# Kernel tuning notes

Measured on AMD Instinct MI355X. Metric: run time of the kernel, lower is better.

Reference implementation:

```python
import jax, jax.numpy as jnp
import numpy as np

NUM_HEADS = 12
TOP_K = 2
ROPE_THETA = 10000.0
EPS = 1e-6

def _rmsnorm(x, w):
    return x * jax.lax.rsqrt(jnp.mean(x * x, axis=-1, keepdims=True) + EPS) * w

def _rotate_half(t):
    t1, t2 = jnp.split(t, 2, axis=-1)
    return jnp.concatenate([-t2, t1], axis=-1)

def setup_inputs() -> dict:
    key = jax.random.key(0)
    ks = jax.random.split(key, 8)
    B, S, H, E, F = 2, 2048, 768, 8, 3072
    s = 0.02
    return {
        "x": jax.random.normal(ks[0], (B, S, H), dtype=jnp.float32),
        "attn_norm_w": jnp.ones((H,), dtype=jnp.float32),
        "wqkv": jax.random.normal(ks[1], (H, 3 * H), dtype=jnp.float32) * s,
        "wo": jax.random.normal(ks[2], (H, H), dtype=jnp.float32) * s,
        "ffn_norm_w": jnp.ones((H,), dtype=jnp.float32),
        "router_w": jax.random.normal(ks[3], (H, E), dtype=jnp.float32) * s,
        "w1": jax.random.normal(ks[4], (E, H, F), dtype=jnp.float32) * s,
        "w2": jax.random.normal(ks[5], (E, F, H), dtype=jnp.float32) * s,
    }

def reference(x, attn_norm_w, wqkv, wo, ffn_norm_w, router_w, w1, w2):
    B, S, H = x.shape
    NH, Dh = NUM_HEADS, H // NUM_HEADS
    E = router_w.shape[1]

    # ---- attention sub-block: x = x + attn(rmsnorm(x)) ----
    h = _rmsnorm(x, attn_norm_w)
    qkv = h @ wqkv  # (B,S,3H)
    q, k, v = [t.reshape(B, S, NH, Dh) for t in jnp.split(qkv, 3, axis=-1)]

    # RoPE (llama-style half-split rotation)
    half = Dh // 2
    inv_freq = 1.0 / (ROPE_THETA ** (jnp.arange(half, dtype=jnp.float32) / half))
    ang = jnp.arange(S, dtype=jnp.float32)[:, None] * inv_freq[None, :]  # (S, half)
    cos = jnp.concatenate([jnp.cos(ang)] * 2, axis=-1)[None, :, None, :].astype(x.dtype)
    sin = jnp.concatenate([jnp.sin(ang)] * 2, axis=-1)[None, :, None, :].astype(x.dtype)
    q = q * cos + _rotate_half(q) * sin
    k = k * cos + _rotate_half(k) * sin

    scores = jnp.einsum('bqhd,bkhd->bhqk', q, k) / jnp.sqrt(jnp.asarray(Dh, x.dtype))
    causal = jnp.tril(jnp.ones((S, S), dtype=bool))
    scores = jnp.where(causal[None, None], scores, jnp.asarray(-1e9, x.dtype))
    attn = jax.nn.softmax(scores, axis=-1)
    o = jnp.einsum('bhqk,bkhd->bqhd', attn, v).reshape(B, S, H) @ wo
    x = x + o

    # ---- MoE FFN sub-block: x = x + moe(rmsnorm(x)) ----
    hn = _rmsnorm(x, ffn_norm_w).reshape(-1, H)  # (T,H)
    logits = hn @ router_w  # (T,E)
    probs = jax.nn.softmax(logits, axis=-1)
    top_v, top_i = jax.lax.top_k(probs, TOP_K)  # (T,K)
    top_v = top_v / jnp.sum(top_v, axis=-1, keepdims=True)
    onehot = jax.nn.one_hot(top_i, E, dtype=x.dtype)  # (T,K,E)
    combine = jnp.einsum('tke,tk->te', onehot, top_v)  # (T,E)

    h1 = jnp.einsum('th,ehf->etf', hn, w1)
    h2 = jnp.einsum('etf,efh->eth', jax.nn.silu(h1), w2)
    moe_out = jnp.einsum('eth,te->th', h2, combine).reshape(B, S, H)

    # load-balancing aux loss (switch-style)
    frac = jnp.mean(jnp.sum(onehot, axis=1), axis=0) / TOP_K  # (E,)
    mean_prob = jnp.mean(probs, axis=0)  # (E,)
    aux = jnp.asarray(E, x.dtype) * jnp.sum(frac * mean_prob)

    return (x + moe_out, aux)
```

## Files before the change

### kernel.cpp

```cpp
#include <hip/hip_runtime.h>
#include <cstdint>
#include <cstddef>

typedef __bf16 bf16;
typedef bf16 bf16x8 __attribute__((ext_vector_type(8)));
typedef bf16 bf16x4 __attribute__((ext_vector_type(4)));
typedef float f32x4 __attribute__((ext_vector_type(4)));

static constexpr size_t SKS = (size_t)10240 * 768;

template <int N> struct ICst { static constexpr int v = N; };

__device__ __forceinline__ void async_cp16(const void* g, void* l) {
    __builtin_amdgcn_global_load_lds(
        (const __attribute__((address_space(1))) unsigned int*)(unsigned long long)g,
        (__attribute__((address_space(3))) unsigned int*)(unsigned int)(unsigned long long)l,
        16, 0, 0);
}

#define BARX() __builtin_amdgcn_s_barrier()
#define LGKM0() asm volatile("s_waitcnt lgkmcnt(0)" ::: "memory")
#define VMC8() asm volatile("s_waitcnt vmcnt(8)" ::: "memory")
#define VMC0() asm volatile("s_waitcnt vmcnt(0)" ::: "memory")

__device__ __forceinline__ void tc_body(const float* __restrict__ in, bf16* __restrict__ out,
                                        int R, int C, int r0, int c0, float* shf) {
    float (*tile)[33] = (float(*)[33])shf;
    int tid = threadIdx.x;
    int lr = tid >> 3, lc = (tid & 7) * 4;
    float4 v = *(const float4*)&in[(size_t)(r0 + lr) * C + c0 + lc];
    tile[lr][lc] = v.x; tile[lr][lc + 1] = v.y; tile[lr][lc + 2] = v.z; tile[lr][lc + 3] = v.w;
    __syncthreads();
    int sc = tid >> 3, sr = (tid & 7) * 4;
    bf16x4 o;
    o[0] = (bf16)tile[sr][sc]; o[1] = (bf16)tile[sr + 1][sc];
    o[2] = (bf16)tile[sr + 2][sc]; o[3] = (bf16)tile[sr + 3][sc];
    *(bf16x4*)&out[(size_t)(c0 + sc) * R + r0 + sr] = o;
}

__global__ __launch_bounds__(256) void prep1(const float* __restrict__ x,
                                             const float* __restrict__ anw,
                                             bf16* __restrict__ hbuf,
                                             const float* __restrict__ wqkv,
                                             bf16* __restrict__ wqkvT,
                                             const float* __restrict__ wo,
                                             bf16* __restrict__ woT,
                                             int* __restrict__ ctrl) {
    __shared__ __align__(16) float shf[32 * 33];
    const int bid = (int)blockIdx.x, tid = threadIdx.x;
    if (bid < 4096) {
        const float* xr = x + (size_t)bid * 768;
        float v0 = xr[tid], v1 = xr[tid + 256], v2 = xr[tid + 512];
        float s = v0 * v0 + v1 * v1 + v2 * v2;
#pragma unroll
        for (int off = 32; off; off >>= 1) s += __shfl_xor(s, off, 64);
        if ((tid & 63) == 0) shf[tid >> 6] = s;
        __syncthreads();
        float tot = shf[0] + shf[1] + shf[2] + shf[3];
        float rs = rsqrtf(tot * (1.f / 768.f) + 1e-6f);
        bf16* o = hbuf + (size_t)bid * 768;
        o[tid]       = (bf16)(v0 * rs * anw[tid]);
        o[tid + 256] = (bf16)(v1 * rs * anw[tid + 256]);
        o[tid + 512] = (bf16)(v2 * rs * anw[tid + 512]);
    } else if (bid < 5824) {
        int i = bid - 4096;
        tc_body(wqkv, wqkvT, 768, 2304, (i / 72) * 32, (i % 72) * 32, shf);
    } else if (bid < 6400) {
        int i = bid - 5824;
        tc_body(wo, woT, 768, 768, (i / 24) * 32, (i % 24) * 32, shf);
    } else {
        if (tid < 64) ctrl[tid] = 0;
    }
}

__global__ __launch_bounds__(256) void rope_kernel(const bf16* __restrict__ qkv,
                                                   bf16* __restrict__ qb,
                                                   bf16* __restrict__ kb,
                                                   bf16* __restrict__ vtb) {
    __shared__ float vs[64][65];
    const int tid = threadIdx.x;
    const int s0 = blockIdx.x * 64, bh = blockIdx.y;
    const int b = bh / 12, h = bh - b * 12;
    const float qscale = 0.18033688f;
#pragma unroll
    for (int i = 0; i < 16; ++i) {
        int idx = i * 256 + tid;
        int sl = idx >> 6, d = idx & 63;
        int sg = s0 + sl;
        size_t base = ((size_t)b * 2048 + sg) * 2304;
        float qv = (float)qkv[base + h * 64 + d];
        float kv = (float)qkv[base + 768 + h * 64 + d];
        float vv = (float)qkv[base + 1536 + h * 64 + d];
        float qp = (float)qkv[base + h * 64 + (d ^ 32)];
        float kp = (float)qkv[base + 768 + h * 64 + (d ^ 32)];
        int jj = d & 31;
        float invf = __expf(-(float)jj * (9.210340371976184f / 32.f));
        float ang = (float)sg * invf;
        float cv, sv;
        __sincosf(ang, &sv, &cv);
        float rq = (d < 32) ? -qp : qp;
        float rk = (d < 32) ? -kp : kp;
        qb[((size_t)bh * 2048 + sg) * 64 + d] = (bf16)((qv * cv + rq * sv) * qscale);
        kb[((size_t)bh * 2048 + sg) * 64 + d] = (bf16)(kv * cv + rk * sv);
        vs[sl][d] = vv;
    }
    __syncthreads();
#pragma unroll
    for (int i = 0; i < 16; ++i) {
        int idx = i * 256 + tid;
        int d = idx >> 6, sl = idx & 63;
        vtb[(size_t)bh * 64 * 2048 + (size_t)d * 2048 + s0 + sl] = (bf16)vs[sl][d];
    }
}

struct AttnSh {
    bf16 Qs[2][64][32];
    bf16 Ks[2][2][64][32];
    bf16 Vts[2][2][64][32];
    bf16 Ps[4][1024];
};
union ShU { AttnSh a; float tile[32 * 33]; };

__global__ __launch_bounds__(256) void attn_tw(const bf16* __restrict__ qb,
                                               const bf16* __restrict__ kb,
                                               const bf16* __restrict__ vtb,
                                               bf16* __restrict__ ob,
                                               const float* __restrict__ w1,
                                               bf16* __restrict__ w1T,
                                               const float* __restrict__ w2,
                                               bf16* __restrict__ w2T) {
    __shared__ __align__(16) ShU sh;
    const int bid = (int)blockIdx.x;

    if (bid >= 768) {
        int i = bid - 768;
        if (i < 18432) {
            int bz = i / 2304, r = i - bz * 2304;
            tc_body(w1 + (size_t)bz * 768 * 3072, w1T + (size_t)bz * 768 * 3072,
                    768, 3072, ((r / 96) % 24) * 32, (r % 96) * 32, sh.tile);
        } else {
            i -= 18432;
            int bz = i / 2304, r = i - bz * 2304;
            tc_body(w2 + (size_t)bz * 3072 * 768, w2T + (size_t)bz * 3072 * 768,
                    3072, 768, ((r / 24) % 96) * 32, (r % 24) * 32, sh.tile);
        }
        return;
    }

    const int tid = threadIdx.x, lane = tid & 63, w = tid >> 6;
    const int quad = lane >> 4, l16 = lane & 15;
    const int linear = bid;
    const int xcd = linear & 7, j = linear >> 3;
    const int bh = xcd * 3 + (j >> 5);
    const int qt = 31 - (j & 31);
    const int q0 = qt * 64;
    const int b = bh / 12, h = bh - b * 12;

    const bf16* qhead = qb + (size_t)bh * 2048 * 64;
    const bf16* khead = kb + (size_t)bh * 2048 * 64;
    const bf16* vthead = vtb + (size_t)bh * 64 * 2048;

#pragma unroll
    for (int i = 0; i < 2; ++i) {
        int o = (i * 256 + tid) * 16;
        int kk = o >> 12, row = (o >> 6) & 63, el = (o & 63) >> 1;
        async_cp16(qhead + (size_t)(q0 + row) * 64 + kk * 32 + el,
                   (char*)sh.a.Qs + (size_t)(i * 256 + w * 64) * 16);
    }
    __syncthreads();
    bf16x8 bq[2];
#pragma unroll
    for (int kk = 0; kk < 2; ++kk)
        bq[kk] = *(const bf16x8*)&sh.a.Qs[kk][w * 16 + l16][quad * 8];

    f32x4 o_acc[4] = {};
    float m_st = -1e30f, l_st = 0.f;

    for (int j2 = 0; j2 <= qt; j2 += 2) {
        int nt2 = (j2 + 1 <= qt) ? 2 : 1;
        __syncthreads();
#pragma unroll
        for (int t = 0; t < 2; ++t) {
            if (t >= nt2) break;
            int kv0 = (j2 + t) * 64;
#pragma unroll
            for (int i = 0; i < 2; ++i) {
                int o = (i * 256 + tid) * 16;
                int kk = o >> 12, row = (o >> 6) & 63, el = (o & 63) >> 1;
                async_cp16(khead + (size_t)(kv0 + row) * 64 + kk * 32 + el,
                           (char*)&sh.a.Ks[t] + (size_t)(i * 256 + w * 64) * 16);
                async_cp16(vthead + (size_t)row * 2048 + kv0 + kk * 32 + el,
                           (char*)&sh.a.Vts[t] + (size_t)(i * 256 + w * 64) * 16);
            }
        }
        __syncthreads();

#pragma unroll
        for (int t = 0; t < 2; ++t) {
            if (t >= nt2) break;

            f32x4 sacc[4] = {};
#pragma unroll
            for (int kk = 0; kk < 2; ++kk) {
                bf16x8 ak[4];
#pragma unroll
                for (int ni = 0; ni < 4; ++ni)
                    ak[ni] = *(const bf16x8*)&sh.a.Ks[t][kk][ni * 16 + l16][quad * 8];
#pragma unroll
                for (int ni = 0; ni < 4; ++ni)
                    sacc[ni] = __builtin_amdgcn_mfma_f32_16x16x32_bf16(ak[ni], bq[kk], sacc[ni], 0, 0, 0);
            }

            if (j2 + t == qt) {
                int ql = w * 16 + l16;
#pragma unroll
                for (int ni = 0; ni < 4; ++ni)
#pragma unroll
                    for (int r = 0; r < 4; ++r)
                        if (ni * 16 + quad * 4 + r > ql) sacc[ni][r] = -1e30f;
            }

            float mx = sacc[0][0];
#pragma unroll
            for (int ni = 0; ni < 4; ++ni)
#pragma unroll
                for (int r = 0; r < 4; ++r) mx = fmaxf(mx, sacc[ni][r]);
            mx = fmaxf(mx, __shfl_xor(mx, 16, 64));
            mx = fmaxf(mx, __shfl_xor(mx, 32, 64));
            float mnew = fmaxf(m_st, mx);
            float alpha = exp2f(m_st - mnew);
            m_st = mnew;
            float rsum = 0.f;
#pragma unroll
            for (int ni = 0; ni < 4; ++ni)
#pragma unroll
                for (int r = 0; r < 4; ++r) {
                    float pv = exp2f(sacc[ni][r] - mnew);
                    sacc[ni][r] = pv;
                    rsum += pv;
                }
            rsum += __shfl_xor(rsum, 16, 64);
            rsum += __shfl_xor(rsum, 32, 64);
            l_st = l_st * alpha + rsum;

            float af[4];
#pragma unroll
            for (int r = 0; r < 4; ++r) af[r] = __shfl(alpha, quad * 4 + r, 64);
#pragma unroll
            for (int ni = 0; ni < 4; ++ni)
#pragma unroll
                for (int r = 0; r < 4; ++r) o_acc[ni][r] *= af[r];

            bf16* pb = sh.a.Ps[w];
#pragma unroll
            for (int ni = 0; ni < 4; ++ni)
#pragma unroll
                for (int r = 0; r < 4; ++r) {
                    int kv = ni * 16 + quad * 4 + r;
                    int ch = (kv >> 3) ^ (l16 & 7);
                    pb[l16 * 64 + ch * 8 + (kv & 7)] = (bf16)sacc[ni][r];
                }

#pragma unroll
            for (int kk = 0; kk < 2; ++kk) {
                int ch = (kk * 4 + quad) ^ (l16 & 7);
                bf16x8 ap = *(const bf16x8*)&pb[l16 * 64 + ch * 8];
                bf16x8 bv[4];
#pragma unroll
                for (int ni = 0; ni < 4; ++ni)
                    bv[ni] = *(const bf16x8*)&sh.a.Vts[t][kk][ni * 16 + l16][quad * 8];
#pragma unroll
                for (int ni = 0; ni < 4; ++ni)
                    o_acc[ni] = __builtin_amdgcn_mfma_f32_16x16x32_bf16(ap, bv[ni], o_acc[ni], 0, 0, 0);
            }
        }
    }

    float lf[4];
#pragma unroll
    for (int r = 0; r < 4; ++r) lf[r] = 1.f / __shfl(l_st, quad * 4 + r, 64);
#pragma unroll
    for (int ni = 0; ni < 4; ++ni)
#pragma unroll
        for (int r = 0; r < 4; ++r) {
            int rowg = q0 + w * 16 + quad * 4 + r;
            size_t tk = (size_t)b * 2048 + rowg;
            ob[tk * 768 + h * 64 + ni * 16 + l16] = (bf16)(o_acc[ni][r] * lf[r]);
        }
}

__global__ __launch_bounds__(256) void rms_router(const float* __restrict__ x1,
                                                  const float* __restrict__ w,
                                                  const float* __restrict__ rw,
                                                  bf16* __restrict__ hn,
                                                  int* __restrict__ topi,
                                                  float* __restrict__ topw,
                                                  float* __restrict__ probsb) {
    __shared__ float hnf[768];
    __shared__ float part[256];
    __shared__ float lg[8];
    __shared__ float probs[8];
    __shared__ float red[4];
    int row = blockIdx.x, tid = threadIdx.x;
    const float* xr = x1 + (size_t)row * 768;
    float v0 = xr[tid], v1 = xr[tid + 256], v2 = xr[tid + 512];
    float s = v0 * v0 + v1 * v1 + v2 * v2;
#pragma unroll
    for (int off = 32; off; off >>= 1) s += __shfl_xor(s, off, 64);
    if ((tid & 63) == 0) red[tid >> 6] = s;
    __syncthreads();
    float tot = red[0] + red[1] + red[2] + red[3];
    float rs = rsqrtf(tot * (1.f / 768.f) + 1e-6f);
    float h0 = v0 * rs * w[tid], h1v = v1 * rs * w[tid + 256], h2v = v2 * rs * w[tid + 512];
    hnf[tid] = h0; hnf[tid + 256] = h1v; hnf[tid + 512] = h2v;
    bf16* o = hn + (size_t)row * 768;
    o[tid] = (bf16)h0; o[tid + 256] = (bf16)h1v; o[tid + 512] = (bf16)h2v;
    __syncthreads();
    int e = tid & 7, seg = tid >> 3;
    float p = 0.f;
#pragma unroll
    for (int j = 0; j < 24; ++j) { int k = seg * 24 + j; p += hnf[k] * rw[k * 8 + e]; }
    part[tid] = p;
    __syncthreads();
    if (tid < 8) { float a = 0.f; for (int sgi = 0; sgi < 32; ++sgi) a += part[sgi * 8 + tid]; lg[tid] = a; }
    __syncthreads();
    if (tid == 0) {
        float mx = lg[0];
        for (int i = 1; i < 8; ++i) mx = fmaxf(mx, lg[i]);
        float ssum = 0.f, ex[8];
        for (int i = 0; i < 8; ++i) { ex[i] = __expf(lg[i] - mx); ssum += ex[i]; }
        float inv = 1.f / ssum;
        for (int i = 0; i < 8; ++i) probs[i] = ex[i] * inv;
        int e0 = 0; float p0 = probs[0];
        for (int i = 1; i < 8; ++i) if (probs[i] > p0) { p0 = probs[i]; e0 = i; }
        int e1 = -1; float p1 = -1.f;
        for (int i = 0; i < 8; ++i) if (i != e0 && probs[i] > p1) { p1 = probs[i]; e1 = i; }
        float wsum = p0 + p1;
        topi[row * 2] = e0; topi[row * 2 + 1] = e1;
        topw[row * 2] = p0 / wsum; topw[row * 2 + 1] = p1 / wsum;
    }
    __syncthreads();
    if (tid < 8) probsb[(size_t)row * 8 + tid] = probs[tid];
}

__global__ __launch_bounds__(256) void router_stats(const float* __restrict__ probsb,
                                                    const int* __restrict__ topi,
                                                    int* ctrl, int4* tiles, float* auxOut) {
    __shared__ float pws[4][8];
    __shared__ int cws[4][8];
    int tid = threadIdx.x;
    float s[8] = {};
    int cnt[8] = {};
    for (int t = tid; t < 4096; t += 256) {
        const float4* p = (const float4*)(probsb + (size_t)t * 8);
        float4 a = p[0], b = p[1];
        s[0] += a.x; s[1] += a.y; s[2] += a.z; s[3] += a.w;
        s[4] += b.x; s[5] += b.y; s[6] += b.z; s[7] += b.w;
        int e0 = topi[2 * t], e1 = topi[2 * t + 1];
#pragma unroll
        for (int e = 0; e < 8; ++e) cnt[e] += (e == e0) + (e == e1);
    }
#pragma unroll
    for (int e = 0; e < 8; ++e)
#pragma unroll
        for (int off = 32; off; off >>= 1) {
            s[e] += __shfl_xor(s[e], off, 64);
            cnt[e] += __shfl_xor(cnt[e], off, 64);
        }
    if ((tid & 63) == 0) {
#pragma unroll
        for (int e = 0; e < 8; ++e) { pws[tid >> 6][e] = s[e]; cws[tid >> 6][e] = cnt[e]; }
    }
    __syncthreads();
    if (tid == 0) {
        int off = 0, nt = 0;
        float aux = 0.f;
        for (int e = 0; e < 8; ++e) {
            int ne = cws[0][e] + cws[1][e] + cws[2][e] + cws[3][e];
            float ps = pws[0][e] + pws[1][e] + pws[2][e] + pws[3][e];
            ctrl[e] = ne;
            ctrl[32 + e] = off;
            int ntl = (ne + 255) >> 8;
            for (int i = 0; i < ntl; ++i) { tiles[nt] = make_int4(e, off + i * 256, off + ne, 0); ++nt; }
            off += ntl << 8;
            aux += ((float)ne * (1.f / 8192.f)) * (ps * (1.f / 4096.f));
        }
        ctrl[24] = nt;
        auxOut[0] = 8.f * aux;
    }
}

__global__ __launch_bounds__(256) void place_tokens(const int* __restrict__ topi,
                                                    int* ctrl, int* __restrict__ perm,
                                                    int* __restrict__ tokslot) {
    __shared__ int lcnt[8], lbase[8];
    int tid = threadIdx.x;
    int t = blockIdx.x * 256 + tid;
    if (tid < 8) lcnt[tid] = 0;
    __syncthreads();
    int e0 = topi[2 * t], e1 = topi[2 * t + 1];
    int p0 = atomicAdd(&lcnt[e0], 1);
    int p1 = atomicAdd(&lcnt[e1], 1);
    __syncthreads();
    if (tid < 8) lbase[tid] = atomicAdd(&ctrl[16 + tid], lcnt[tid]);
    __syncthreads();
    int g0 = ctrl[32 + e0] + lbase[e0] + p0;
    int g1 = ctrl[32 + e1] + lbase[e1] + p1;
    perm[g0] = t; perm[g1] = t;
    tokslot[2 * t] = g0; tokslot[2 * t + 1] = g1;
}

__global__ __launch_bounds__(192) void moe_combine(const float* __restrict__ h2p,
                                                   const int* __restrict__ tokslot,
                                                   const float* __restrict__ topw,
                                                   float* __restrict__ out) {
    int t = blockIdx.x, tid = threadIdx.x;
    int s0 = tokslot[2 * t], s1 = tokslot[2 * t + 1];
    float w0 = topw[2 * t], w1 = topw[2 * t + 1];
    int c = tid * 4;
    float4 a0 = *(const float4*)(h2p + (size_t)s0 * 768 + c);
    float4 a1 = *(const float4*)(h2p + SKS + (size_t)s0 * 768 + c);
    float4 b0 = *(const float4*)(h2p + (size_t)s1 * 768 + c);
    float4 b1 = *(const float4*)(h2p + SKS + (size_t)s1 * 768 + c);
    float4* o = (float4*)(out + (size_t)t * 768 + c);
    float4 ov = *o;
    ov.x += w0 * (a0.x + a1.x) + w1 * (b0.x + b1.x);
    ov.y += w0 * (a0.y + a1.y) + w1 * (b0.y + b1.y);
    ov.z += w0 * (a0.z + a1.z) + w1 * (b0.z + b1.z);
    ov.w += w0 * (a0.w + a1.w) + w1 * (b0.w + b1.w);
    *o = ov;
}

template <int MODE, int KTOT, int SK>
__global__ __launch_bounds__(512, 2) void gemm8p(const bf16* __restrict__ A,
                                                 const bf16* __restrict__ Bt,
                                                 int N,
                                                 bf16* __restrict__ outB,
                                                 float* __restrict__ outF,
                                                 const int4* __restrict__ tiles,
                                                 const int* __restrict__ ctrl,
                                                 const int* __restrict__ perm) {
    constexpr int KB = KTOT / SK;
    constexpr int nT = KB >> 6;
    __shared__ __align__(16) bf16 As[2][2][128 * 64];
    __shared__ __align__(16) bf16 Bs[2][2][128 * 64];
    __shared__ int sPerm[256];

    const int tid = threadIdx.x, lane = tid & 63, wid = tid >> 6;
    const int wr = wid >> 2, wc = wid & 3;
    const int quad = lane >> 4, l16 = lane & 15;

    const int NB = N >> 8;
    const int nwg = (int)gridDim.x, q8 = nwg >> 3;
    const int L = (int)blockIdx.x;
    const int lin = (L & 7) * q8 + (L >> 3);
    int mt, nb, sk = 0;
    if (SK == 2) { int d = NB * 2; mt = lin / d; int r = lin - mt * d; nb = r >> 1; sk = r & 1; }
    else         { mt = lin / NB; nb = lin - mt * NB; }
    const int n0 = nb << 8;
    const int k0 = sk * KB;

    int m0 = 0, row0 = 0;
    if (MODE == 0) {
        m0 = mt << 8;
    } else {
        if (mt >= ctrl[24]) return;
        int4 td = tiles[mt];
        row0 = td.y;
        Bt += (size_t)td.x * (size_t)N * KTOT;
        if (MODE == 2) {
            if (tid < 256) {
                int g = row0 + tid;
                sPerm[tid] = perm[(g < td.z) ? g : row0];
            }
            __syncthreads();
        }
    }

    const int r0t = tid >> 3, s0t = tid & 7;
    const int cOff = ((s0t ^ (r0t & 7)) << 3);
    unsigned aOff[2][2], bOff[2][2];
#pragma unroll
    for (int h = 0; h < 2; ++h)
#pragma unroll
        for (int i = 0; i < 2; ++i) {
            int rrow = h * 128 + i * 64 + r0t;
            bOff[h][i] = (unsigned)((((n0 + rrow) * KTOT) + k0 + cOff) * 2);
            int ar = (MODE == 0) ? (m0 + rrow) : (MODE == 2 ? sPerm[rrow] : row0 + rrow);
            aOff[h][i] = (unsigned)(((ar * KTOT) + k0 + cOff) * 2);
        }
    const char* Ab = (const char*)A;
    const char* Bb = (const char*)Bt;

    auto stA = [&](int buf, int ktB) {
#pragma unroll
        for (int h = 0; h < 2; ++h)
#pragma unroll
            for (int i = 0; i < 2; ++i)
                async_cp16(Ab + aOff[h][i] + ktB,
                           (char*)As[buf][h] + (size_t)((i * 512 + wid * 64) * 16));
    };
    auto stB = [&](int buf, int ktB) {
#pragma unroll
        for (int h = 0; h < 2; ++h)
#pragma unroll
            for (int i = 0; i < 2; ++i)
                async_cp16(Bb + bOff[h][i] + ktB,
                           (char*)Bs[buf][h] + (size_t)((i * 512 + wid * 64) * 16));
    };

    const bf16* aP[2][2];
    const bf16* bP[2][2];
#pragma unroll
    for (int bb = 0; bb < 2; ++bb)
#pragma unroll
        for (int kk = 0; kk < 2; ++kk) {
            int swz = ((kk * 4 + quad) ^ (l16 & 7)) * 8;
            aP[bb][kk] = (const bf16*)As[bb][wr] + l16 * 64 + swz;
            bP[bb][kk] = (const bf16*)Bs[bb][wc >> 1] + ((wc & 1) * 64 + l16) * 64 + swz;
        }

    f32x4 acc[8][4] = {};
    bf16x8 aLo[4][2], aHi[4][2], bLo[2][2], bHi[2][2];

    stA(0, 0); stB(0, 0); stA(1, 128); stB(1, 128);
    VMC8();
    BARX();

    auto dotile = [&](auto BC, int t) {
        constexpr int b = decltype(BC)::v;
        const bool st = (t + 2 < nT);
        const int ktB = (t + 2) << 7;

#pragma unroll
        for (int mi = 0; mi < 4; ++mi) {
            aLo[mi][0] = *(const bf16x8*)(aP[b][0] + mi * 1024);
            aLo[mi][1] = *(const bf16x8*)(aP[b][1] + mi * 1024);
        }
#pragma unroll
        for (int ni = 0; ni < 2; ++ni) {
            bLo[ni][0] = *(const bf16x8*)(bP[b][0] + ni * 1024);
            bLo[ni][1] = *(const bf16x8*)(bP[b][1] + ni * 1024);
        }
        BARX(); LGKM0();
        __builtin_amdgcn_s_setprio(1);
#pragma unroll
        for (int mi = 0; mi < 4; ++mi)
#pragma unroll
            for (int ni = 0; ni < 2; ++ni) {
                acc[mi][ni] = __builtin_amdgcn_mfma_f32_16x16x32_bf16(aLo[mi][0], bLo[ni][0], acc[mi][ni], 0, 0, 0);
                acc[mi][ni] = __builtin_amdgcn_mfma_f32_16x16x32_bf16(aLo[mi][1], bLo[ni][1], acc[mi][ni], 0, 0, 0);
            }
        __builtin_amdgcn_s_setprio(0);
        BARX();

#pragma unroll
        for (int ni = 0; ni < 2; ++ni) {
            bHi[ni][0] = *(const bf16x8*)(bP[b][0] + (ni + 2) * 1024);
            bHi[ni][1] = *(const bf16x8*)(bP[b][1] + (ni + 2) * 1024);
        }
        BARX(); LGKM0();
        __builtin_amdgcn_s_setprio(1);
#pragma unroll
        for (int mi = 0; mi < 4; ++mi)
#pragma unroll
            for (int ni = 0; ni < 2; ++ni) {
                acc[mi][ni + 2] = __builtin_amdgcn_mfma_f32_16x16x32_bf16(aLo[mi][0], bHi[ni][0], acc[mi][ni + 2], 0, 0, 0);
                acc[mi][ni + 2] = __builtin_amdgcn_mfma_f32_16x16x32_bf16(aLo[mi][1], bHi[ni][1], acc[mi][ni + 2], 0, 0, 0);
            }
        __builtin_amdgcn_s_setprio(0);
        BARX();

#pragma unroll
        for (int mi = 0; mi < 4; ++mi) {
            aHi[mi][0] = *(const bf16x8*)(aP[b][0] + (mi + 4) * 1024);
            aHi[mi][1] = *(const bf16x8*)(aP[b][1] + (mi + 4) * 1024);
        }
        if (st) stB(b, ktB);
        BARX(); LGKM0();
        __builtin_amdgcn_s_setprio(1);
#pragma unroll
        for (int mi = 0; mi < 4; ++mi)
#pragma unroll
            for (int ni = 0; ni < 2; ++ni) {
                acc[mi + 4][ni + 2] = __builtin_amdgcn_mfma_f32_16x16x32_bf16(aHi[mi][0], bHi[ni][0], acc[mi + 4][ni + 2], 0, 0, 0);
                acc[mi + 4][ni + 2] = __builtin_amdgcn_mfma_f32_16x16x32_bf16(aHi[mi][1], bHi[ni][1], acc[mi + 4][ni + 2], 0, 0, 0);
            }
        __builtin_amdgcn_s_setprio(0);
        BARX();

        if (st) stA(b, ktB);
        BARX();
        __builtin_amdgcn_s_setprio(1);
#pragma unroll
        for (int mi = 0; mi < 4; ++mi)
#pragma unroll
            for (int ni = 0; ni < 2; ++ni) {
                acc[mi + 4][ni] = __builtin_amdgcn_mfma_f32_16x16x32_bf16(aHi[mi][0], bLo[ni][0], acc[mi + 4][ni], 0, 0, 0);
                acc[mi + 4][ni] = __builtin_amdgcn_mfma_f32_16x16x32_bf16(aHi[mi][1], bLo[ni][1], acc[mi + 4][ni], 0, 0, 0);
            }
        __builtin_amdgcn_s_setprio(0);
        if (st) { VMC8(); } else if (t + 2 == nT) { VMC0(); }
        BARX();
    };

    for (int t = 0; t < nT; t += 2) {
        dotile(ICst<0>{}, t);
        dotile(ICst<1>{}, t + 1);
    }

#pragma unroll
    for (int mi = 0; mi < 8; ++mi)
#pragma unroll
        for (int ni = 0; ni < 4; ++ni)
#pragma unroll
            for (int r = 0; r < 4; ++r) {
                int lrow = wr * 128 + mi * 16 + quad * 4 + r;
                int col  = n0 + wc * 64 + ni * 16 + l16;
                float v = acc[mi][ni][r];
                if (MODE == 0) {
                    outB[(size_t)(m0 + lrow) * N + col] = (bf16)v;
                } else if (MODE == 2) {
                    float sv = v / (1.f + __expf(-v));
                    outB[(size_t)(row0 + lrow) * N + col] = (bf16)sv;
                } else {
                    outF[(size_t)sk * SKS + (size_t)(row0 + lrow) * N + col] = v;
                }
            }
}

template <int MODE, int NBX, int MTX>
__global__ __launch_bounds__(256) void gemm_nt(const bf16* __restrict__ A,
                                               const bf16* __restrict__ Bt,
                                               int N, int K,
                                               const float* __restrict__ xres,
                                               float* __restrict__ outF,
                                               bf16* __restrict__ outB) {
    __shared__ __align__(16) bf16 As[2][128 * 32];
    __shared__ __align__(16) bf16 Bs[2][128 * 32];

    const int tid = threadIdx.x, lane = tid & 63, w = tid >> 6;
    const int wr = w >> 1, wc = w & 1, quad = lane >> 4, l16 = lane & 15;

    const int L = blockIdx.x;
    const int xcd = L & 7, j = L >> 3;
    const int mt = xcd * MTX + j / NBX;
    const int n0 = (j % NBX) * 128;
    const int m0 = mt * 128;

    auto stage = [&](int buf, int kt) {
#pragma unroll
        for (int i = 0; i < 2; ++i) {
            int c = i * 256 + tid;
            int r = c >> 2, koff = (c & 3) * 8;
            async_cp16(A + (size_t)(m0 + r) * K + kt + koff,
                       (char*)As[buf] + (size_t)(i * 256 + w * 64) * 16);
            async_cp16(Bt + (size_t)(n0 + r) * K + kt + koff,
                       (char*)Bs[buf] + (size_t)(i * 256 + w * 64) * 16);
        }
    };

    f32x4 acc[4][4] = {};
    const int nIt = K >> 5;
    stage(0, 0);

    for (int it = 0; it < nIt; ++it) {
        const int cur = it & 1;
        __syncthreads();
        if (it + 1 < nIt) stage(cur ^ 1, (it + 1) << 5);

        bf16x8 af[4], bfr[4];
#pragma unroll
        for (int mi = 0; mi < 4; ++mi)
            af[mi] = *(const bf16x8*)(As[cur] + (wr * 64 + mi * 16 + l16) * 32 + quad * 8);
#pragma unroll
        for (int ni = 0; ni < 4; ++ni)
            bfr[ni] = *(const bf16x8*)(Bs[cur] + (wc * 64 + ni * 16 + l16) * 32 + quad * 8);
#pragma unroll
        for (int mi = 0; mi < 4; ++mi)
#pragma unroll
            for (int ni = 0; ni < 4; ++ni)
                acc[mi][ni] = __builtin_amdgcn_mfma_f32_16x16x32_bf16(af[mi], bfr[ni], acc[mi][ni], 0, 0, 0);
    }

#pragma unroll
    for (int mi = 0; mi < 4; ++mi)
#pragma unroll
        for (int ni = 0; ni < 4; ++ni)
#pragma unroll
            for (int r = 0; r < 4; ++r) {
                int lrow = wr * 64 + mi * 16 + quad * 4 + r;
                int col = n0 + wc * 64 + ni * 16 + l16;
                float v = acc[mi][ni][r];
                if (MODE == 1) {
                    size_t idx = (size_t)(m0 + lrow) * N + col;
                    outF[idx] = v + xres[idx];
                } else {
                    outB[(size_t)(m0 + lrow) * N + col] = (bf16)v;
                }
            }
}

extern "C" void kernel_launch(void* const* d_in, const int* in_sizes, int n_in,
                              void* d_out, int out_size, void* d_ws, size_t ws_size,
                              hipStream_t stream) {
    const float* x    = (const float*)d_in[0];
    const float* anw  = (const float*)d_in[1];
    const float* wqkv = (const float*)d_in[2];
    const float* wo   = (const float*)d_in[3];
    const float* fnw  = (const float*)d_in[4];
    const float* rw   = (const float*)d_in[5];
    const float* w1   = (const float*)d_in[6];
    const float* w2   = (const float*)d_in[7];
    float* out = (float*)d_out;

    char* ws = (char*)d_ws;
    size_t off = 0;
    auto alloc = [&](size_t bytes) -> char* {
        char* p = ws + off;
        off = (off + bytes + 255) & ~(size_t)255;
        return p;
    };
    bf16* wqkvT = (bf16*)alloc(2304ull * 768 * 2);
    bf16* woT   = (bf16*)alloc(768ull * 768 * 2);
    bf16* w2T   = (bf16*)alloc(8ull * 768 * 3072 * 2);
    bf16* w1T   = (bf16*)alloc(8ull * 3072 * 768 * 2);
    bf16* hbuf  = (bf16*)alloc(4096ull * 768 * 2);
    bf16* qkvb  = (bf16*)alloc(4096ull * 2304 * 2);
    bf16* qb    = (bf16*)alloc(24ull * 2048 * 64 * 2);
    bf16* kb    = (bf16*)alloc(24ull * 2048 * 64 * 2);
    bf16* vtb   = (bf16*)alloc(24ull * 64 * 2048 * 2);
    bf16* obuf  = (bf16*)alloc(4096ull * 768 * 2);
    bf16* hn    = (bf16*)alloc(4096ull * 768 * 2);
    int*  topi  = (int*)alloc(4096ull * 2 * 4);
    float* topw = (float*)alloc(4096ull * 2 * 4);
    float* probsb = (float*)alloc(4096ull * 8 * 4);
    int*  ctrl  = (int*)alloc(64 * 4);
    int4* tiles = (int4*)alloc(80 * 16);
    int*  perm  = (int*)alloc(10240 * 4);
    int*  tokslot = (int*)alloc(4096ull * 2 * 4);
    bf16* h1    = (bf16*)alloc(10240ull * 3072 * 2);
    float* h2p  = (float*)w1T;
    (void)ws_size; (void)in_sizes; (void)n_in;

    prep1<<<6401, 256, 0, stream>>>(x, anw, hbuf, wqkv, wqkvT, wo, woT, ctrl);
    gemm8p<0, 768, 1><<<144, 512, 0, stream>>>(hbuf, wqkvT, 2304, qkvb, nullptr,
                                               nullptr, nullptr, nullptr);
    rope_kernel<<<dim3(32, 24), 256, 0, stream>>>(qkvb, qb, kb, vtb);
    attn_tw<<<768 + 36864, 256, 0, stream>>>(qb, kb, vtb, obuf, w1, w1T, w2, w2T);
    gemm_nt<1, 6, 4><<<192, 256, 0, stream>>>(obuf, woT, 768, 768, x, out, nullptr);
    rms_router<<<4096, 256, 0, stream>>>(out, fnw, rw, hn, topi, topw, probsb);
    router_stats<<<1, 256, 0, stream>>>(probsb, topi, ctrl, tiles, out + (out_size - 1));
    place_tokens<<<16, 256, 0, stream>>>(topi, ctrl, perm, tokslot);
    gemm8p<2, 768, 1><<<480, 512, 0, stream>>>(hn, w1T, 3072, h1, nullptr,
                                               tiles, ctrl, perm);
    gemm8p<3, 3072, 2><<<240, 512, 0, stream>>>(h1, w2T, 768, nullptr, h2p,
                                                tiles, ctrl, perm);
    moe_combine<<<4096, 192, 0, stream>>>(h2p, tokslot, topw, out);
}
```

Before: 449.1 us.

## Halve GEMM K-tile to raise occupancy, add nontemporal weight loads and attention priority

The main GEMM kernel's K tile per stage drops from 64 to 32, which halves LDS use. The swizzle, async-copy offsets and fragment loads are reworked to match, and launch bounds move from 2 to 4 blocks per CU so more waves can hide latency. The MoE weight transpose now reads w1/w2 with nontemporal loads to reduce cache pollution. Attention blocks raise wave priority over the co-scheduled transpose blocks. In exchange there are twice as many K iterations, with more barriers and waitcnt stalls per unit of work, and the register budget per thread is tighter.

```diff
diff --git a/kernel.cpp b/kernel.cpp
--- a/kernel.cpp
+++ b/kernel.cpp
@@ -20,16 +20,18 @@
 
 #define BARX() __builtin_amdgcn_s_barrier()
 #define LGKM0() asm volatile("s_waitcnt lgkmcnt(0)" ::: "memory")
-#define VMC8() asm volatile("s_waitcnt vmcnt(8)" ::: "memory")
+#define VMC4() asm volatile("s_waitcnt vmcnt(4)" ::: "memory")
 #define VMC0() asm volatile("s_waitcnt vmcnt(0)" ::: "memory")
 
+template <bool NTLD>
 __device__ __forceinline__ void tc_body(const float* __restrict__ in, bf16* __restrict__ out,
                                         int R, int C, int r0, int c0, float* shf) {
     float (*tile)[33] = (float(*)[33])shf;
     int tid = threadIdx.x;
     int lr = tid >> 3, lc = (tid & 7) * 4;
-    float4 v = *(const float4*)&in[(size_t)(r0 + lr) * C + c0 + lc];
-    tile[lr][lc] = v.x; tile[lr][lc + 1] = v.y; tile[lr][lc + 2] = v.z; tile[lr][lc + 3] = v.w;
+    const f32x4* gp = (const f32x4*)&in[(size_t)(r0 + lr) * C + c0 + lc];
+    f32x4 v = NTLD ? __builtin_nontemporal_load(gp) : *gp;
+    tile[lr][lc] = v[0]; tile[lr][lc + 1] = v[1]; tile[lr][lc + 2] = v[2]; tile[lr][lc + 3] = v[3];
     __syncthreads();
     int sc = tid >> 3, sr = (tid & 7) * 4;
     bf16x4 o;
@@ -64,10 +66,10 @@
         o[tid + 512] = (bf16)(v2 * rs * anw[tid + 512]);
     } else if (bid < 5824) {
         int i = bid - 4096;
-        tc_body(wqkv, wqkvT, 768, 2304, (i / 72) * 32, (i % 72) * 32, shf);
+        tc_body<false>(wqkv, wqkvT, 768, 2304, (i / 72) * 32, (i % 72) * 32, shf);
     } else if (bid < 6400) {
         int i = bid - 5824;
-        tc_body(wo, woT, 768, 768, (i / 24) * 32, (i % 24) * 32, shf);
+        tc_body<false>(wo, woT, 768, 768, (i / 24) * 32, (i % 24) * 32, shf);
     } else {
         if (tid < 64) ctrl[tid] = 0;
     }
@@ -136,16 +138,18 @@
         int i = bid - 768;
         if (i < 18432) {
             int bz = i / 2304, r = i - bz * 2304;
-            tc_body(w1 + (size_t)bz * 768 * 3072, w1T + (size_t)bz * 768 * 3072,
-                    768, 3072, ((r / 96) % 24) * 32, (r % 96) * 32, sh.tile);
+            tc_body<true>(w1 + (size_t)bz * 768 * 3072, w1T + (size_t)bz * 768 * 3072,
+                          768, 3072, ((r / 96) % 24) * 32, (r % 96) * 32, sh.tile);
         } else {
             i -= 18432;
             int bz = i / 2304, r = i - bz * 2304;
-            tc_body(w2 + (size_t)bz * 3072 * 768, w2T + (size_t)bz * 3072 * 768,
-                    3072, 768, ((r / 24) % 96) * 32, (r % 24) * 32, sh.tile);
+            tc_body<true>(w2 + (size_t)bz * 3072 * 768, w2T + (size_t)bz * 3072 * 768,
+                          3072, 768, ((r / 24) % 96) * 32, (r % 24) * 32, sh.tile);
         }
         return;
     }
+
+    __builtin_amdgcn_s_setprio(1);
 
     const int tid = threadIdx.x, lane = tid & 63, w = tid >> 6;
     const int quad = lane >> 4, l16 = lane & 15;
@@ -287,6 +291,7 @@
             size_t tk = (size_t)b * 2048 + rowg;
             ob[tk * 768 + h * 64 + ni * 16 + l16] = (bf16)(o_acc[ni][r] * lf[r]);
         }
+    __builtin_amdgcn_s_setprio(0);
 }
 
 __global__ __launch_bounds__(256) void rms_router(const float* __restrict__ x1,
@@ -432,7 +437,7 @@
 }
 
 template <int MODE, int KTOT, int SK>
-__global__ __launch_bounds__(512, 2) void gemm8p(const bf16* __restrict__ A,
+__global__ __launch_bounds__(512, 4) void gemm8p(const bf16* __restrict__ A,
                                                  const bf16* __restrict__ Bt,
                                                  int N,
                                                  bf16* __restrict__ outB,
@@ -441,9 +446,9 @@
                                                  const int* __restrict__ ctrl,
                                                  const int* __restrict__ perm) {
     constexpr int KB = KTOT / SK;
-    constexpr int nT = KB >> 6;
-    __shared__ __align__(16) bf16 As[2][2][128 * 64];
-    __shared__ __align__(16) bf16 Bs[2][2][128 * 64];
+    constexpr int nT = KB >> 5;
+    __shared__ __align__(16) bf16 As[2][2][128 * 32];
+    __shared__ __align__(16) bf16 Bs[2][2][128 * 32];
     __shared__ int sPerm[256];
 
     const int tid = threadIdx.x, lane = tid & 63, wid = tid >> 6;
@@ -477,130 +482,78 @@
         }
     }
 
-    const int r0t = tid >> 3, s0t = tid & 7;
-    const int cOff = ((s0t ^ (r0t & 7)) << 3);
-    unsigned aOff[2][2], bOff[2][2];
-#pragma unroll
-    for (int h = 0; h < 2; ++h)
-#pragma unroll
-        for (int i = 0; i < 2; ++i) {
-            int rrow = h * 128 + i * 64 + r0t;
-            bOff[h][i] = (unsigned)((((n0 + rrow) * KTOT) + k0 + cOff) * 2);
-            int ar = (MODE == 0) ? (m0 + rrow) : (MODE == 2 ? sPerm[rrow] : row0 + rrow);
-            aOff[h][i] = (unsigned)(((ar * KTOT) + k0 + cOff) * 2);
-        }
+    const int r0t = tid >> 2, s0t = tid & 3;
+    const int cOff = ((s0t ^ (r0t & 3) ^ ((r0t >> 2) & 3)) << 3);
+    unsigned aOff[2], bOff[2];
+#pragma unroll
+    for (int h = 0; h < 2; ++h) {
+        int rrow = h * 128 + r0t;
+        bOff[h] = (unsigned)((((n0 + rrow) * KTOT) + k0 + cOff) * 2);
+        int ar = (MODE == 0) ? (m0 + rrow) : (MODE == 2 ? sPerm[rrow] : row0 + rrow);
+        aOff[h] = (unsigned)(((ar * KTOT) + k0 + cOff) * 2);
+    }
     const char* Ab = (const char*)A;
     const char* Bb = (const char*)Bt;
 
     auto stA = [&](int buf, int ktB) {
 #pragma unroll
         for (int h = 0; h < 2; ++h)
-#pragma unroll
-            for (int i = 0; i < 2; ++i)
-                async_cp16(Ab + aOff[h][i] + ktB,
-                           (char*)As[buf][h] + (size_t)((i * 512 + wid * 64) * 16));
+            async_cp16(Ab + aOff[h] + ktB, (char*)As[buf][h] + (size_t)tid * 16);
     };
     auto stB = [&](int buf, int ktB) {
 #pragma unroll
         for (int h = 0; h < 2; ++h)
-#pragma unroll
-            for (int i = 0; i < 2; ++i)
-                async_cp16(Bb + bOff[h][i] + ktB,
-                           (char*)Bs[buf][h] + (size_t)((i * 512 + wid * 64) * 16));
+            async_cp16(Bb + bOff[h] + ktB, (char*)Bs[buf][h] + (size_t)tid * 16);
     };
 
-    const bf16* aP[2][2];
-    const bf16* bP[2][2];
-#pragma unroll
-    for (int bb = 0; bb < 2; ++bb)
-#pragma unroll
-        for (int kk = 0; kk < 2; ++kk) {
-            int swz = ((kk * 4 + quad) ^ (l16 & 7)) * 8;
-            aP[bb][kk] = (const bf16*)As[bb][wr] + l16 * 64 + swz;
-            bP[bb][kk] = (const bf16*)Bs[bb][wc >> 1] + ((wc & 1) * 64 + l16) * 64 + swz;
-        }
+    const int rswz = ((quad ^ (l16 & 3) ^ ((l16 >> 2) & 3)) << 3);
+    const bf16* aP[2];
+    const bf16* bP[2];
+#pragma unroll
+    for (int bb = 0; bb < 2; ++bb) {
+        aP[bb] = (const bf16*)As[bb][wr] + l16 * 32 + rswz;
+        bP[bb] = (const bf16*)Bs[bb][wc >> 1] + ((wc & 1) * 64 + l16) * 32 + rswz;
+    }
 
     f32x4 acc[8][4] = {};
-    bf16x8 aLo[4][2], aHi[4][2], bLo[2][2], bHi[2][2];
-
-    stA(0, 0); stB(0, 0); stA(1, 128); stB(1, 128);
-    VMC8();
+    bf16x8 aLo[4], aHi[4], bF[4];
+
+    stA(0, 0); stB(0, 0); stA(1, 64); stB(1, 64);
+    VMC4();
     BARX();
 
     auto dotile = [&](auto BC, int t) {
         constexpr int b = decltype(BC)::v;
         const bool st = (t + 2 < nT);
-        const int ktB = (t + 2) << 7;
-
-#pragma unroll
-        for (int mi = 0; mi < 4; ++mi) {
-            aLo[mi][0] = *(const bf16x8*)(aP[b][0] + mi * 1024);
-            aLo[mi][1] = *(const bf16x8*)(aP[b][1] + mi * 1024);
-        }
-#pragma unroll
-        for (int ni = 0; ni < 2; ++ni) {
-            bLo[ni][0] = *(const bf16x8*)(bP[b][0] + ni * 1024);
-            bLo[ni][1] = *(const bf16x8*)(bP[b][1] + ni * 1024);
-        }
+        const int ktB = (t + 2) << 6;
+
+#pragma unroll
+        for (int mi = 0; mi < 4; ++mi) aLo[mi] = *(const bf16x8*)(aP[b] + mi * 512);
+#pragma unroll
+        for (int ni = 0; ni < 4; ++ni) bF[ni] = *(const bf16x8*)(bP[b] + ni * 512);
         BARX(); LGKM0();
         __builtin_amdgcn_s_setprio(1);
 #pragma unroll
         for (int mi = 0; mi < 4; ++mi)
 #pragma unroll
-            for (int ni = 0; ni < 2; ++ni) {
-                acc[mi][ni] = __builtin_amdgcn_mfma_f32_16x16x32_bf16(aLo[mi][0], bLo[ni][0], acc[mi][ni], 0, 0, 0);
-                acc[mi][ni] = __builtin_amdgcn_mfma_f32_16x16x32_bf16(aLo[mi][1], bLo[ni][1], acc[mi][ni], 0, 0, 0);
-            }
+            for (int ni = 0; ni < 4; ++ni)
+                acc[mi][ni] = __builtin_amdgcn_mfma_f32_16x16x32_bf16(aLo[mi], bF[ni], acc[mi][ni], 0, 0, 0);
         __builtin_amdgcn_s_setprio(0);
         BARX();
 
 #pragma unroll
-        for (int ni = 0; ni < 2; ++ni) {
-            bHi[ni][0] = *(const bf16x8*)(bP[b][0] + (ni + 2) * 1024);
-            bHi[ni][1] = *(const bf16x8*)(bP[b][1] + (ni + 2) * 1024);
-        }
-        BARX(); LGKM0();
-        __builtin_amdgcn_s_setprio(1);
-#pragma unroll
-        for (int mi = 0; mi < 4; ++mi)
-#pragma unroll
-            for (int ni = 0; ni < 2; ++ni) {
-                acc[mi][ni + 2] = __builtin_amdgcn_mfma_f32_16x16x32_bf16(aLo[mi][0], bHi[ni][0], acc[mi][ni + 2], 0, 0, 0);
-                acc[mi][ni + 2] = __builtin_amdgcn_mfma_f32_16x16x32_bf16(aLo[mi][1], bHi[ni][1], acc[mi][ni + 2], 0, 0, 0);
-            }
-        __builtin_amdgcn_s_setprio(0);
-        BARX();
-
-#pragma unroll
-        for (int mi = 0; mi < 4; ++mi) {
-            aHi[mi][0] = *(const bf16x8*)(aP[b][0] + (mi + 4) * 1024);
-            aHi[mi][1] = *(const bf16x8*)(aP[b][1] + (mi + 4) * 1024);
-        }
+        for (int mi = 0; mi < 4; ++mi) aHi[mi] = *(const bf16x8*)(aP[b] + (mi + 4) * 512);
         if (st) stB(b, ktB);
         BARX(); LGKM0();
         __builtin_amdgcn_s_setprio(1);
 #pragma unroll
         for (int mi = 0; mi < 4; ++mi)
 #pragma unroll
-            for (int ni = 0; ni < 2; ++ni) {
-                acc[mi + 4][ni + 2] = __builtin_amdgcn_mfma_f32_16x16x32_bf16(aHi[mi][0], bHi[ni][0], acc[mi + 4][ni + 2], 0, 0, 0);
-                acc[mi + 4][ni + 2] = __builtin_amdgcn_mfma_f32_16x16x32_bf16(aHi[mi][1], bHi[ni][1], acc[mi + 4][ni + 2], 0, 0, 0);
-            }
+            for (int ni = 0; ni < 4; ++ni)
+                acc[mi + 4][ni] = __builtin_amdgcn_mfma_f32_16x16x32_bf16(aHi[mi], bF[ni], acc[mi + 4][ni], 0, 0, 0);
         __builtin_amdgcn_s_setprio(0);
-        BARX();
-
         if (st) stA(b, ktB);
-        BARX();
-        __builtin_amdgcn_s_setprio(1);
-#pragma unroll
-        for (int mi = 0; mi < 4; ++mi)
-#pragma unroll
-            for (int ni = 0; ni < 2; ++ni) {
-                acc[mi + 4][ni] = __builtin_amdgcn_mfma_f32_16x16x32_bf16(aHi[mi][0], bLo[ni][0], acc[mi + 4][ni], 0, 0, 0);
-                acc[mi + 4][ni] = __builtin_amdgcn_mfma_f32_16x16x32_bf16(aHi[mi][1], bLo[ni][1], acc[mi + 4][ni], 0, 0, 0);
-            }
-        __builtin_amdgcn_s_setprio(0);
-        if (st) { VMC8(); } else if (t + 2 == nT) { VMC0(); }
+        if (st) { VMC4(); } else if (t + 2 == nT) { VMC0(); }
         BARX();
     };
 
```

After: 1.333 ms. +196.7%, slower.
